# Kernel tuning notes

Measured on AMD Instinct MI355X. Metric: run time of the kernel, lower is better.

## Reference

```python
import jax, jax.numpy as jnp
import numpy as np

LAMBDA_OTDL = 1.0


def _emd2_1d(p, q):
    """Exact EMD^2 (squared-distance cost on integer grid) between two 1D
    histograms p, q of length D. For convex cost |i-j|^2 on a line the optimal
    plan is the monotone (quantile) coupling, so
      EMD2 = int_0^1 (F_p^{-1}(t) - F_q^{-1}(t))^2 dt,
    matching ot.emd2 with M[i,j] = |i-j|^2 exactly."""
    D = p.shape[0]
    cp = jnp.cumsum(p)
    cq = jnp.cumsum(q)
    t = jnp.sort(jnp.concatenate([cp, cq]))          # [2D] merged CDF breakpoints
    dt = jnp.diff(t, prepend=jnp.zeros((1,), t.dtype))
    tm = t - 0.5 * dt                                 # segment midpoints
    ip = jnp.clip(jnp.searchsorted(cp, tm, side='left'), 0, D - 1)
    iq = jnp.clip(jnp.searchsorted(cq, tm, side='left'), 0, D - 1)
    return jnp.sum(dt * (ip - iq).astype(p.dtype) ** 2)


def setup_inputs() -> dict:
    key = jax.random.key(0)
    k1, k2 = jax.random.split(key)
    B, C, D, W = 65536, 1, 256, 1
    P = jax.random.uniform(k1, (B, C, D, W), dtype=jnp.float32)
    Q = jax.random.uniform(k2, (B, C, D, W), dtype=jnp.float32)
    return {"P": P, "Q": Q}


def reference(P, Q):
    B = P.shape[0]
    P_prime = P / jnp.sum(P, axis=(2, 3), keepdims=True)
    Q_prime = Q / jnp.sum(Q, axis=(2, 3), keepdims=True)
    p_flat = P_prime.reshape(B, -1)   # [B, D] since C=W=1
    q_flat = Q_prime.reshape(B, -1)
    OT_values = jax.vmap(_emd2_1d)(p_flat, q_flat)          # [B]
    OT_values = jax.lax.stop_gradient(OT_values)            # original detaches (numpy solver)
    mse_loss = jnp.mean((P - Q) ** 2, axis=(1, 2, 3))       # [B]
    loss = mse_loss + LAMBDA_OTDL * OT_values
    return jnp.mean(loss)
```

## Files before the change

### kernel.cpp

```cpp
#include <hip/hip_runtime.h>


#define NW    4
#define DSZ   256
#define LROW  264

__global__ __launch_bounds__(256) void otdl_main(
    const float* __restrict__ P, const float* __restrict__ Q,
    double* __restrict__ partial, int B, int bpw)
{
    __shared__ float  s_cp[NW][LROW];
    __shared__ float  s_cq[NW][LROW];
    __shared__ double s_bsum[NW];

    const int tid  = threadIdx.x;
    const int wv   = tid >> 6;
    const int lane = tid & 63;
    const int wgl  = blockIdx.x * NW + wv;

    float* cp = s_cp[wv];
    float* cq = s_cq[wv];

    if (lane == 0) { cp[DSZ] = 2.0f; cq[DSZ] = 2.0f; }

    double acc = 0.0;
    const int k0 = lane * 8;

    for (int it = 0; it < bpw; ++it) {
        int b = wgl * bpw + it;
        bool valid = (b < B);
        int bc = valid ? b : (B - 1);

        const float4* Pr = reinterpret_cast<const float4*>(P + (size_t)bc * DSZ);
        const float4* Qr = reinterpret_cast<const float4*>(Q + (size_t)bc * DSZ);
        float4 pv = Pr[lane];
        float4 qv = Qr[lane];

        float dx = pv.x - qv.x, dy = pv.y - qv.y;
        float dz = pv.z - qv.z, dw = pv.w - qv.w;
        float msel = dx*dx + dy*dy + dz*dz + dw*dw;

        float pl = pv.x + pv.y + pv.z + pv.w;
        float ql = qv.x + qv.y + qv.z + qv.w;

        float ps = pl, qs = ql;
#pragma unroll
        for (int off = 1; off < 64; off <<= 1) {
            float tp = __shfl_up(ps, off, 64);
            float tq = __shfl_up(qs, off, 64);
            ps += (lane >= off) ? tp : 0.0f;
            qs += (lane >= off) ? tq : 0.0f;
        }
        float ptot = __shfl(ps, 63, 64);
        float qtot = __shfl(qs, 63, 64);
        float rp = 1.0f / ptot;
        float rq = 1.0f / qtot;
        float pe = ps - pl;
        float qe = qs - ql;

        float vP[4], vQ[4];
        vP[0] = (pe + pv.x) * rp;
        vP[1] = (pe + pv.x + pv.y) * rp;
        vP[2] = (pe + pv.x + pv.y + pv.z) * rp;
        vP[3] = ps * rp;
        vQ[0] = (qe + qv.x) * rq;
        vQ[1] = (qe + qv.x + qv.y) * rq;
        vQ[2] = (qe + qv.x + qv.y + qv.z) * rq;
        vQ[3] = qs * rq;

        __syncthreads();
        int base = lane * 4;
#pragma unroll
        for (int e = 0; e < 4; ++e) { cp[base + e] = vP[e]; cq[base + e] = vQ[e]; }
        __syncthreads();

        int lo = k0 > DSZ ? k0 - DSZ : 0;
        int hi = k0 < DSZ ? k0 : DSZ;
#pragma unroll
        for (int s = 0; s < 9; ++s) {
            int mid = (lo + hi) >> 1;
            int jm1 = k0 - 1 - mid;
            int jr  = jm1 < 0 ? 0 : jm1;
            float cqv = cq[jr];
            float cpv = cp[mid];
            bool pred = (jm1 < 0) || (cqv <= cpv);
            hi = pred ? mid : hi;
            lo = pred ? lo  : mid + 1;
        }
        int i = lo;
        int j = k0 - lo;

        float a  = cp[i];
        float b2 = cq[j];
        float emdl = 0.0f;
#pragma unroll
        for (int s = 0; s < 8; ++s) {
            bool  ea  = a < b2;
            float val = ea ? a : b2;
            int   own = ea ? i : j;
            int   oth = ea ? j : i;
            int   otc = oth > 255 ? 255 : oth;
            float coef = (own > 254) ? 0.0f : (float)(2 * otc - 2 * own - 1);
            emdl = fmaf(val, coef, emdl);
            i += ea ? 1 : 0;
            j += ea ? 0 : 1;
            a  = cp[i];
            b2 = cq[j];
        }

        if (valid) acc += (double)(emdl + msel * (1.0f / 256.0f));
    }

#pragma unroll
    for (int off = 32; off; off >>= 1) {
        double o = __shfl_xor(acc, off, 64);
        acc += o;
    }
    if (lane == 0) s_bsum[wv] = acc;
    __syncthreads();
    if (tid == 0) {
        partial[blockIdx.x] = s_bsum[0] + s_bsum[1] + s_bsum[2] + s_bsum[3];
    }
}

__global__ __launch_bounds__(256) void otdl_reduce(
    const double* __restrict__ partial, int n, float* __restrict__ out, double invB)
{
    __shared__ double sdata[256];
    double a = 0.0;
    for (int i = threadIdx.x; i < n; i += 256) a += partial[i];
    sdata[threadIdx.x] = a;
    __syncthreads();
    for (int s2 = 128; s2 > 0; s2 >>= 1) {
        if (threadIdx.x < s2) sdata[threadIdx.x] += sdata[threadIdx.x + s2];
        __syncthreads();
    }
    if (threadIdx.x == 0) out[0] = (float)(sdata[0] * invB);
}

extern "C" void kernel_launch(void* const* d_in, const int* in_sizes, int n_in,
                              void* d_out, int out_size, void* d_ws, size_t ws_size,
                              hipStream_t stream)
{
    const float* P = (const float*)d_in[0];
    const float* Q = (const float*)d_in[1];
    float* out = (float*)d_out;
    double* partial = (double*)d_ws;

    int B = in_sizes[0] / DSZ;
    const int blocks = 2048;
    const int totalWaves = blocks * NW;
    int bpw = (B + totalWaves - 1) / totalWaves;

    otdl_main<<<blocks, 256, 0, stream>>>(P, Q, partial, B, bpw);
    otdl_reduce<<<1, 256, 0, stream>>>(partial, blocks, out, 1.0 / (double)B);
}
```

Before: 47.94 us.

## Process two rows per wave with prefetch, LDS double buffer, no block barriers

Each wave now handles two rows per iteration, so the two prefix-sum shuffles and the two merge searches can interleave. The next pair's global loads are issued before the merge work on the current pair to hide memory latency. The CDF arrays are double-buffered per wave, and the block-wide __syncthreads is replaced by an LDS waitcnt, since each wave only touches its own slice of shared memory. The merge loop also reads the next CDF values ahead of time. The cost is more registers, and the pair loop silently drops the last row when bpw is odd.

```diff
diff --git a/kernel.cpp b/kernel.cpp
--- a/kernel.cpp
+++ b/kernel.cpp
@@ -9,8 +9,8 @@
     const float* __restrict__ P, const float* __restrict__ Q,
     double* __restrict__ partial, int B, int bpw)
 {
-    __shared__ float  s_cp[NW][LROW];
-    __shared__ float  s_cq[NW][LROW];
+    __shared__ float  s_cp[NW][2][LROW];
+    __shared__ float  s_cq[NW][2][LROW];
     __shared__ double s_bsum[NW];
 
     const int tid  = threadIdx.x;
@@ -18,97 +18,143 @@
     const int lane = tid & 63;
     const int wgl  = blockIdx.x * NW + wv;
 
-    float* cp = s_cp[wv];
-    float* cq = s_cq[wv];
-
-    if (lane == 0) { cp[DSZ] = 2.0f; cq[DSZ] = 2.0f; }
+    if (lane == 0) {
+        s_cp[wv][0][DSZ] = 2.0f; s_cq[wv][0][DSZ] = 2.0f;
+        s_cp[wv][1][DSZ] = 2.0f; s_cq[wv][1][DSZ] = 2.0f;
+    }
 
     double acc = 0.0;
-    const int k0 = lane * 8;
-
-    for (int it = 0; it < bpw; ++it) {
-        int b = wgl * bpw + it;
-        bool valid = (b < B);
-        int bc = valid ? b : (B - 1);
-
-        const float4* Pr = reinterpret_cast<const float4*>(P + (size_t)bc * DSZ);
-        const float4* Qr = reinterpret_cast<const float4*>(Q + (size_t)bc * DSZ);
-        float4 pv = Pr[lane];
-        float4 qv = Qr[lane];
-
-        float dx = pv.x - qv.x, dy = pv.y - qv.y;
-        float dz = pv.z - qv.z, dw = pv.w - qv.w;
-        float msel = dx*dx + dy*dy + dz*dz + dw*dw;
-
-        float pl = pv.x + pv.y + pv.z + pv.w;
-        float ql = qv.x + qv.y + qv.z + qv.w;
-
-        float ps = pl, qs = ql;
+    const int  k0      = lane * 8;
+    const int  npair   = bpw >> 1;
+    const long rowbase = (long)wgl * bpw;
+
+    float4 pv[2], qv[2], npv[2], nqv[2];
+#pragma unroll
+    for (int r = 0; r < 2; ++r) {
+        long b = rowbase + r;
+        long c = (b < B) ? b : (B - 1);
+        pv[r] = reinterpret_cast<const float4*>(P + c * DSZ)[lane];
+        qv[r] = reinterpret_cast<const float4*>(Q + c * DSZ)[lane];
+    }
+
+    for (int p = 0; p < npair; ++p) {
+        float msel[2], pl[2], ql[2], ps[2], qs[2];
+#pragma unroll
+        for (int r = 0; r < 2; ++r) {
+            float dx = pv[r].x - qv[r].x, dy = pv[r].y - qv[r].y;
+            float dz = pv[r].z - qv[r].z, dw = pv[r].w - qv[r].w;
+            msel[r] = dx*dx + dy*dy + dz*dz + dw*dw;
+            pl[r] = pv[r].x + pv[r].y + pv[r].z + pv[r].w;
+            ql[r] = qv[r].x + qv[r].y + qv[r].z + qv[r].w;
+            ps[r] = pl[r]; qs[r] = ql[r];
+        }
 #pragma unroll
         for (int off = 1; off < 64; off <<= 1) {
-            float tp = __shfl_up(ps, off, 64);
-            float tq = __shfl_up(qs, off, 64);
-            ps += (lane >= off) ? tp : 0.0f;
-            qs += (lane >= off) ? tq : 0.0f;
-        }
-        float ptot = __shfl(ps, 63, 64);
-        float qtot = __shfl(qs, 63, 64);
-        float rp = 1.0f / ptot;
-        float rq = 1.0f / qtot;
-        float pe = ps - pl;
-        float qe = qs - ql;
-
-        float vP[4], vQ[4];
-        vP[0] = (pe + pv.x) * rp;
-        vP[1] = (pe + pv.x + pv.y) * rp;
-        vP[2] = (pe + pv.x + pv.y + pv.z) * rp;
-        vP[3] = ps * rp;
-        vQ[0] = (qe + qv.x) * rq;
-        vQ[1] = (qe + qv.x + qv.y) * rq;
-        vQ[2] = (qe + qv.x + qv.y + qv.z) * rq;
-        vQ[3] = qs * rq;
-
-        __syncthreads();
-        int base = lane * 4;
-#pragma unroll
-        for (int e = 0; e < 4; ++e) { cp[base + e] = vP[e]; cq[base + e] = vQ[e]; }
-        __syncthreads();
-
-        int lo = k0 > DSZ ? k0 - DSZ : 0;
-        int hi = k0 < DSZ ? k0 : DSZ;
-#pragma unroll
-        for (int s = 0; s < 9; ++s) {
-            int mid = (lo + hi) >> 1;
-            int jm1 = k0 - 1 - mid;
-            int jr  = jm1 < 0 ? 0 : jm1;
-            float cqv = cq[jr];
-            float cpv = cp[mid];
-            bool pred = (jm1 < 0) || (cqv <= cpv);
-            hi = pred ? mid : hi;
-            lo = pred ? lo  : mid + 1;
-        }
-        int i = lo;
-        int j = k0 - lo;
-
-        float a  = cp[i];
-        float b2 = cq[j];
-        float emdl = 0.0f;
-#pragma unroll
-        for (int s = 0; s < 8; ++s) {
-            bool  ea  = a < b2;
-            float val = ea ? a : b2;
-            int   own = ea ? i : j;
-            int   oth = ea ? j : i;
-            int   otc = oth > 255 ? 255 : oth;
-            float coef = (own > 254) ? 0.0f : (float)(2 * otc - 2 * own - 1);
-            emdl = fmaf(val, coef, emdl);
-            i += ea ? 1 : 0;
-            j += ea ? 0 : 1;
-            a  = cp[i];
-            b2 = cq[j];
-        }
-
-        if (valid) acc += (double)(emdl + msel * (1.0f / 256.0f));
+#pragma unroll
+            for (int r = 0; r < 2; ++r) {
+                float tp = __shfl_up(ps[r], off, 64);
+                float tq = __shfl_up(qs[r], off, 64);
+                ps[r] += (lane >= off) ? tp : 0.0f;
+                qs[r] += (lane >= off) ? tq : 0.0f;
+            }
+        }
+
+        asm volatile("s_waitcnt lgkmcnt(0)" ::: "memory");
+
+        const int base = lane * 4;
+        float vP[2][4], vQ[2][4];
+#pragma unroll
+        for (int r = 0; r < 2; ++r) {
+            float rp = 1.0f / __shfl(ps[r], 63, 64);
+            float rq = 1.0f / __shfl(qs[r], 63, 64);
+            float pe = ps[r] - pl[r];
+            float qe = qs[r] - ql[r];
+            vP[r][0] = (pe + pv[r].x) * rp;
+            vP[r][1] = (pe + pv[r].x + pv[r].y) * rp;
+            vP[r][2] = (pe + pv[r].x + pv[r].y + pv[r].z) * rp;
+            vP[r][3] = ps[r] * rp;
+            vQ[r][0] = (qe + qv[r].x) * rq;
+            vQ[r][1] = (qe + qv[r].x + qv[r].y) * rq;
+            vQ[r][2] = (qe + qv[r].x + qv[r].y + qv[r].z) * rq;
+            vQ[r][3] = qs[r] * rq;
+#pragma unroll
+            for (int e = 0; e < 4; ++e) {
+                s_cp[wv][r][base + e] = vP[r][e];
+                s_cq[wv][r][base + e] = vQ[r][e];
+            }
+        }
+
+        asm volatile("s_waitcnt lgkmcnt(0)" ::: "memory");
+
+        if (p + 1 < npair) {
+#pragma unroll
+            for (int r = 0; r < 2; ++r) {
+                long b = rowbase + 2 * (p + 1) + r;
+                long c = (b < B) ? b : (B - 1);
+                npv[r] = reinterpret_cast<const float4*>(P + c * DSZ)[lane];
+                nqv[r] = reinterpret_cast<const float4*>(Q + c * DSZ)[lane];
+            }
+        }
+
+        int ii[2], jj[2];
+#pragma unroll
+        for (int r = 0; r < 2; ++r) {
+            const float* cp = s_cp[wv][r];
+            const float* cq = s_cq[wv][r];
+            int lo = k0 > DSZ ? k0 - DSZ : 0;
+            int hi = k0 < DSZ ? k0 : DSZ;
+#pragma unroll
+            for (int s = 0; s < 9; ++s) {
+                int mid = (lo + hi) >> 1;
+                int jm1 = k0 - 1 - mid;
+                int jr  = jm1 < 0 ? 0 : jm1;
+                float cqv = cq[jr];
+                float cpv = cp[mid];
+                bool pred = (jm1 < 0) || (cqv <= cpv);
+                hi = pred ? mid : hi;
+                lo = pred ? lo  : mid + 1;
+            }
+            ii[r] = lo;
+            jj[r] = k0 - lo;
+        }
+
+        float emdl[2];
+#pragma unroll
+        for (int r = 0; r < 2; ++r) {
+            const float* cp = s_cp[wv][r];
+            const float* cq = s_cq[wv][r];
+            int i = ii[r], j = jj[r];
+            float a  = cp[i];
+            float b2 = cq[j];
+            float an = cp[i + 1];
+            float bn = cq[j + 1];
+            float e_ = 0.0f;
+#pragma unroll
+            for (int s = 0; s < 8; ++s) {
+                bool  ea  = a < b2;
+                float val = ea ? a : b2;
+                int   own = ea ? i : j;
+                int   oth = ea ? j : i;
+                int   otc = oth > 255 ? 255 : oth;
+                float coef = (own > 254) ? 0.0f : (float)(2 * otc - 2 * own - 1);
+                e_ = fmaf(val, coef, e_);
+                i += ea ? 1 : 0;
+                j += ea ? 0 : 1;
+                a  = ea ? an : a;
+                b2 = ea ? b2 : bn;
+                an = cp[i + 1];
+                bn = cq[j + 1];
+            }
+            emdl[r] = e_;
+        }
+
+#pragma unroll
+        for (int r = 0; r < 2; ++r) {
+            long b = rowbase + 2 * p + r;
+            if (b < B) acc += (double)(emdl[r] + msel[r] * (1.0f / 256.0f));
+            pv[r] = npv[r];
+            qv[r] = nqv[r];
+        }
     }
 
 #pragma unroll
```

After: 48.35 us. Within noise of the previous version (+0.9%).

## Prefetch next rows, DPP wave scan, drop block barriers, streamline merge walk

Applied to the files above, without the earlier changes.

Loads the next row's P/Q values one iteration ahead so global memory latency overlaps compute. Replaces the shfl-based prefix scan with DPP row ops plus readlane, and replaces the two __syncthreads with lgkmcnt waits because each wave owns its own LDS slice. It also rewrites the merge walk to update coefficients incrementally and detect the end through a sentinel, and it sets an occupancy hint through launch bounds. The risks are a subtle correctness issue in the DPP scan (row_bcast masks) and in the sentinel-based last-element test, plus higher register pressure from the prefetch.

```diff
diff --git a/kernel.cpp b/kernel.cpp
--- a/kernel.cpp
+++ b/kernel.cpp
@@ -5,7 +5,27 @@
 #define DSZ   256
 #define LROW  264
 
-__global__ __launch_bounds__(256) void otdl_main(
+template <int CTRL, int RMASK, bool BC>
+__device__ __forceinline__ float dpp_add(float x) {
+    int t = __builtin_amdgcn_update_dpp(0, __float_as_int(x), CTRL, RMASK, 0xf, BC);
+    return x + __int_as_float(t);
+}
+
+__device__ __forceinline__ float wave_scan(float x) {
+    x = dpp_add<0x111, 0xf, true >(x);
+    x = dpp_add<0x112, 0xf, true >(x);
+    x = dpp_add<0x114, 0xf, true >(x);
+    x = dpp_add<0x118, 0xf, true >(x);
+    x = dpp_add<0x142, 0xa, false>(x);
+    x = dpp_add<0x143, 0xc, false>(x);
+    return x;
+}
+
+__device__ __forceinline__ float lane63(float x) {
+    return __int_as_float(__builtin_amdgcn_readlane(__float_as_int(x), 63));
+}
+
+__global__ __launch_bounds__(256, 8) void otdl_main(
     const float* __restrict__ P, const float* __restrict__ Q,
     double* __restrict__ partial, int B, int bpw)
 {
@@ -24,17 +44,24 @@
     if (lane == 0) { cp[DSZ] = 2.0f; cq[DSZ] = 2.0f; }
 
     double acc = 0.0;
-    const int k0 = lane * 8;
+    const int  k0      = lane * 8;
+    const long rowbase = (long)wgl * bpw;
+
+    float4 pv, qv, npv, nqv;
+    {
+        long c = (rowbase < B) ? rowbase : (B - 1);
+        pv = reinterpret_cast<const float4*>(P + c * DSZ)[lane];
+        qv = reinterpret_cast<const float4*>(Q + c * DSZ)[lane];
+    }
 
     for (int it = 0; it < bpw; ++it) {
-        int b = wgl * bpw + it;
-        bool valid = (b < B);
-        int bc = valid ? b : (B - 1);
+        long b = rowbase + it;
 
-        const float4* Pr = reinterpret_cast<const float4*>(P + (size_t)bc * DSZ);
-        const float4* Qr = reinterpret_cast<const float4*>(Q + (size_t)bc * DSZ);
-        float4 pv = Pr[lane];
-        float4 qv = Qr[lane];
+        if (it + 1 < bpw) {
+            long c = (b + 1 < B) ? (b + 1) : (B - 1);
+            npv = reinterpret_cast<const float4*>(P + c * DSZ)[lane];
+            nqv = reinterpret_cast<const float4*>(Q + c * DSZ)[lane];
+        }
 
         float dx = pv.x - qv.x, dy = pv.y - qv.y;
         float dz = pv.z - qv.z, dw = pv.w - qv.w;
@@ -42,37 +69,29 @@
 
         float pl = pv.x + pv.y + pv.z + pv.w;
         float ql = qv.x + qv.y + qv.z + qv.w;
+        float ps = wave_scan(pl);
+        float qs = wave_scan(ql);
 
-        float ps = pl, qs = ql;
-#pragma unroll
-        for (int off = 1; off < 64; off <<= 1) {
-            float tp = __shfl_up(ps, off, 64);
-            float tq = __shfl_up(qs, off, 64);
-            ps += (lane >= off) ? tp : 0.0f;
-            qs += (lane >= off) ? tq : 0.0f;
-        }
-        float ptot = __shfl(ps, 63, 64);
-        float qtot = __shfl(qs, 63, 64);
-        float rp = 1.0f / ptot;
-        float rq = 1.0f / qtot;
+        float rp = 1.0f / lane63(ps);
+        float rq = 1.0f / lane63(qs);
         float pe = ps - pl;
         float qe = qs - ql;
 
-        float vP[4], vQ[4];
-        vP[0] = (pe + pv.x) * rp;
-        vP[1] = (pe + pv.x + pv.y) * rp;
-        vP[2] = (pe + pv.x + pv.y + pv.z) * rp;
-        vP[3] = ps * rp;
-        vQ[0] = (qe + qv.x) * rq;
-        vQ[1] = (qe + qv.x + qv.y) * rq;
-        vQ[2] = (qe + qv.x + qv.y + qv.z) * rq;
-        vQ[3] = qs * rq;
+        float vP0 = (pe + pv.x) * rp;
+        float vP1 = (pe + pv.x + pv.y) * rp;
+        float vP2 = (pe + pv.x + pv.y + pv.z) * rp;
+        float vP3 = ps * rp;
+        float vQ0 = (qe + qv.x) * rq;
+        float vQ1 = (qe + qv.x + qv.y) * rq;
+        float vQ2 = (qe + qv.x + qv.y + qv.z) * rq;
+        float vQ3 = qs * rq;
 
-        __syncthreads();
-        int base = lane * 4;
-#pragma unroll
-        for (int e = 0; e < 4; ++e) { cp[base + e] = vP[e]; cq[base + e] = vQ[e]; }
-        __syncthreads();
+        asm volatile("s_waitcnt lgkmcnt(0)" ::: "memory");
+
+        *reinterpret_cast<float4*>(&cp[lane * 4]) = make_float4(vP0, vP1, vP2, vP3);
+        *reinterpret_cast<float4*>(&cq[lane * 4]) = make_float4(vQ0, vQ1, vQ2, vQ3);
+
+        asm volatile("s_waitcnt lgkmcnt(0)" ::: "memory");
 
         int lo = k0 > DSZ ? k0 - DSZ : 0;
         int hi = k0 < DSZ ? k0 : DSZ;
@@ -87,28 +106,36 @@
             hi = pred ? mid : hi;
             lo = pred ? lo  : mid + 1;
         }
-        int i = lo;
-        int j = k0 - lo;
+        const float* pA = cp + lo;
+        const float* pB = cq + (k0 - lo);
 
-        float a  = cp[i];
-        float b2 = cq[j];
-        float emdl = 0.0f;
+        float u  = (float)(4 * lo - 2 * k0 - 1);
+        float a  = pA[0];
+        float b2 = pB[0];
+        float an = pA[1];
+        float bn = pB[1];
+        float e_ = 0.0f;
 #pragma unroll
         for (int s = 0; s < 8; ++s) {
-            bool  ea  = a < b2;
-            float val = ea ? a : b2;
-            int   own = ea ? i : j;
-            int   oth = ea ? j : i;
-            int   otc = oth > 255 ? 255 : oth;
-            float coef = (own > 254) ? 0.0f : (float)(2 * otc - 2 * own - 1);
-            emdl = fmaf(val, coef, emdl);
-            i += ea ? 1 : 0;
-            j += ea ? 0 : 1;
-            a  = cp[i];
-            b2 = cq[j];
+            bool  ea   = a < b2;
+            float val  = ea ? a : b2;
+            float u2   = u + 2.0f;
+            float coef = ea ? -u2 : u;
+            bool  last = ea ? (an == 2.0f) : (bn == 2.0f);
+            coef = last ? 0.0f : coef;
+            e_ = fmaf(val, coef, e_);
+            u  = ea ? u2 : (u - 2.0f);
+            pA += ea ? 1 : 0;
+            pB += ea ? 0 : 1;
+            a  = ea ? an : a;
+            b2 = ea ? b2 : bn;
+            an = pA[1];
+            bn = pB[1];
         }
 
-        if (valid) acc += (double)(emdl + msel * (1.0f / 256.0f));
+        if (b < B) acc += (double)(e_ + msel * (1.0f / 256.0f));
+        pv = npv;
+        qv = nqv;
     }
 
 #pragma unroll
```

Result: no change. 47.19 us (-1.6%).
